# Optimization experiments

Hardware: AMD Instinct MI355X
Metric: run time of the kernel (lower is better)

## Reference

```python
import jax, jax.numpy as jnp
import numpy as np

C_IN, C_P1, C_G1, N_OUT = 512, 256, 256, 6
B, H, W = 256, 19, 19


def mish(x):
    return x * jnp.tanh(jax.nn.softplus(x))


def setup_inputs() -> dict:
    key = jax.random.key(0)
    ks = jax.random.split(key, 8)
    x = jax.random.normal(ks[0], (B, C_IN, H, W), dtype=jnp.float32)
    mask = jnp.ones((B, 1, H, W), dtype=jnp.float32)
    conv1p_w = jax.random.normal(ks[1], (C_P1, C_IN), dtype=jnp.float32) * (1.0 / np.sqrt(C_IN))
    conv1g_w = jax.random.normal(ks[2], (C_G1, C_IN), dtype=jnp.float32) * (1.0 / np.sqrt(C_IN))
    beta_g = jnp.zeros((C_G1,), dtype=jnp.float32)
    linear_g_w = jax.random.normal(ks[3], (C_P1, 3 * C_G1), dtype=jnp.float32) * (1.0 / np.sqrt(3 * C_G1))
    beta2 = jnp.zeros((C_P1,), dtype=jnp.float32)
    conv2p_w = jax.random.normal(ks[4], (N_OUT, C_P1), dtype=jnp.float32) * (0.3 / np.sqrt(C_P1))
    return {"x": x, "mask": mask, "conv1p_w": conv1p_w, "conv1g_w": conv1g_w,
            "beta_g": beta_g, "linear_g_w": linear_g_w, "beta2": beta2, "conv2p_w": conv2p_w}


def reference(x, mask, conv1p_w, conv1g_w, beta_g, linear_g_w, beta2, conv2p_w):
    # 1x1 convs are channel GEMMs
    outp = jnp.einsum('bchw,oc->bohw', x, conv1p_w)              # [B, C_P1, H, W]
    outg = jnp.einsum('bchw,oc->bohw', x, conv1g_w)              # [B, C_G1, H, W]
    # BiasMask (scale=None) + Mish
    outg = mish((outg + beta_g[None, :, None, None]) * mask)
    # KataGPool: mean, scaled mean, max (masked)
    mask_sum_hw = jnp.sum(mask, axis=(2, 3), keepdims=True)      # [B,1,1,1]
    layer_mean = jnp.sum(outg * mask, axis=(2, 3), keepdims=True) / mask_sum_hw
    layer_max = jnp.max(outg + (mask - 1.0), axis=(2, 3), keepdims=True)
    sqrt_off = (jnp.sqrt(mask_sum_hw) - 14.0) / 10.0
    pooled = jnp.concatenate([layer_mean, layer_mean * sqrt_off, layer_max], axis=1)  # [B, 3*C_G1, 1, 1]
    pooled = pooled[:, :, 0, 0]                                  # [B, 3*C_G1]
    g = pooled @ linear_g_w.T                                    # [B, C_P1]
    # broadcast-add, BiasMask, Mish
    outp = mish((outp + g[:, :, None, None] + beta2[None, :, None, None]) * mask)
    # final 1x1 conv + invalid-move penalty
    outp = jnp.einsum('bchw,oc->bohw', outp, conv2p_w)           # [B, 6, H, W]
    outp = outp - (1.0 - mask) * 5000.0
    return outp.reshape(outp.shape[0], outp.shape[1], -1)        # [B, 6, H*W]
```

## Files before the change

kernel.cpp:

```cpp
#include <hip/hip_runtime.h>
#include <math.h>

#define BATCH 256
#define CIN   512
#define CP    256
#define HW    361
#define NOUT  6

typedef short bf16x8 __attribute__((ext_vector_type(8)));
typedef float f32x4  __attribute__((ext_vector_type(4)));

__device__ __forceinline__ short f2bf(float f) {
    unsigned u = __float_as_uint(f);
    u += 0x7fffu + ((u >> 16) & 1u);
    return (short)(u >> 16);
}
__device__ __forceinline__ float bf2f(short s) {
    return __uint_as_float(((unsigned)(unsigned short)s) << 16);
}
__device__ __forceinline__ float mish_f(float v) {
    float u = __expf(v);
    float a = 1.f + u;
    float w = a * a;
    float r = v * (w - 1.f) * __builtin_amdgcn_rcpf(w + 1.f);
    return (v > 30.f) ? v : r;
}
__device__ __forceinline__ void gl_lds16(const void* g, void* l) {
    __builtin_amdgcn_global_load_lds(
        (const __attribute__((address_space(1))) void*)g,
        (__attribute__((address_space(3))) void*)l, 16, 0, 0);
}

__global__ __launch_bounds__(256) void k0_weights(
    const float* __restrict__ w1p, const float* __restrict__ w1g,
    short* __restrict__ wT)
{
    int g = blockIdx.x * 256 + threadIdx.x;
    int half = g >> 14;
    int kb   = (g >> 10) & 15;
    int row  = (g >> 2) & 255;
    int s    = g & 3;
    int sc   = s ^ ((row >> 1) & 3);
    const float* src = (half == 0) ? (w1p + (size_t)row * CIN)
                                   : (w1g + (size_t)row * CIN);
    int c = kb * 32 + sc * 8;
    float f[8];
    *(float4*)(f)     = *(const float4*)(src + c);
    *(float4*)(f + 4) = *(const float4*)(src + c + 4);
    bf16x8 v;
    #pragma unroll
    for (int i = 0; i < 8; ++i) v[i] = f2bf(f[i]);
    *(bf16x8*)((char*)wT + (size_t)half * 262144 + kb * 16384 + row * 64 + s * 16) = v;
}

__global__ __launch_bounds__(512, 4) void k1_conv1(
    const float* __restrict__ x, const short* __restrict__ wT,
    const float* __restrict__ mask, const float* __restrict__ beta_g,
    short* __restrict__ outp_pre, float* __restrict__ psum, float* __restrict__ pmax)
{
    int orig = blockIdx.x;
    int newid = (orig & 7) * 192 + (orig >> 3);
    int half = newid & 1;
    int nb = newid >> 1;
    int n = nb % 3;
    int b = nb / 3;

    const int tid = threadIdx.x;
    const int lane = tid & 63, wid = tid >> 6;
    const int wm = wid >> 1, wn = wid & 1;
    const int lc = lane & 15, lg = lane >> 4;
    const int hw0 = n * 128;

    __shared__ __align__(16) short As[3][8192];
    __shared__ __align__(16) short Bs[2][4096];
    __shared__ float maskS[128], betaS[256];
    float* redS = (float*)(&As[0][0]);
    float* redM = redS + 512;

    if (tid < 128) {
        int hwg = hw0 + tid;
        maskS[tid] = (hwg < HW) ? mask[b * HW + hwg] : 0.f;
    }
    if (tid < 256) betaS[tid] = beta_g[tid];
    asm volatile("s_waitcnt vmcnt(0) lgkmcnt(0)" ::: "memory");
    __builtin_amdgcn_sched_barrier(0);

    const int brow = tid & 127;
    const int bs   = tid >> 7;
    const int bsc  = bs ^ ((brow >> 1) & 3);
    const int hwg  = hw0 + brow;
    const bool bvalid = hwg < HW;
    const float* xb = x + ((size_t)b * CIN + bsc * 8) * HW + hwg;
    char* bDstBase = (char*)Bs;

    const char* aSrc = (const char*)wT + (size_t)half * 262144 + tid * 16;
    char* aDst = (char*)As + tid * 16;

    int aOff[4], bOff[4];
    #pragma unroll
    for (int mf = 0; mf < 4; ++mf) {
        int r = wm * 64 + mf * 16 + lc;
        aOff[mf] = r * 64 + ((lg ^ ((r >> 1) & 3)) * 16);
    }
    #pragma unroll
    for (int nf = 0; nf < 4; ++nf) {
        int r = wn * 64 + nf * 16 + lc;
        bOff[nf] = r * 64 + ((lg ^ ((r >> 1) & 3)) * 16);
    }

    float regB[8];
    #pragma unroll
    for (int i = 0; i < 8; ++i) regB[i] = 0.f;

    f32x4 acc[4][4];
    #pragma unroll
    for (int i = 0; i < 4; ++i)
        #pragma unroll
        for (int j = 0; j < 4; ++j)
            acc[i][j] = (f32x4){0.f, 0.f, 0.f, 0.f};

#define BLOAD(kb)                                                          \
    do {                                                                   \
        const float* src_ = xb + (size_t)(kb) * 32 * HW;                   \
        _Pragma("unroll")                                                  \
        for (int i_ = 0; i_ < 8; ++i_) {                                   \
            regB[i_] = bvalid ? src_[(size_t)i_ * HW] : 0.f;               \
        }                                                                  \
    } while (0)

#define BWRITE(buf)                                                        \
    do {                                                                   \
        bf16x8 o_;                                                         \
        _Pragma("unroll")                                                  \
        for (int i_ = 0; i_ < 8; ++i_) o_[i_] = f2bf(regB[i_]);            \
        *(bf16x8*)(bDstBase + (buf) * 8192 + brow * 64 + bs * 16) = o_;    \
    } while (0)

#define ALOAD(buf, kb)                                                     \
    do {                                                                   \
        gl_lds16(aSrc + (kb) * 16384,        aDst + (buf) * 16384);        \
        gl_lds16(aSrc + (kb) * 16384 + 8192, aDst + (buf) * 16384 + 8192); \
    } while (0)

    BLOAD(0); ALOAD(0, 0);
    asm volatile("s_waitcnt vmcnt(2)" ::: "memory");
    __builtin_amdgcn_sched_barrier(0);
    BWRITE(0);
    BLOAD(1); ALOAD(1, 1);
    asm volatile("s_waitcnt vmcnt(10)" ::: "memory");
    __builtin_amdgcn_sched_barrier(0);
    asm volatile("s_waitcnt lgkmcnt(0)" ::: "memory");
    __builtin_amdgcn_s_barrier();
    __builtin_amdgcn_sched_barrier(0);

    #pragma unroll
    for (int t = 0; t < 16; ++t) {
        const int bufA = t % 3;
        const int bufB = t & 1;
        const char* ab = (const char*)As + bufA * 16384;
        const char* bb = (const char*)Bs + bufB * 8192;

        bf16x8 aF[4], bF[4];
        #pragma unroll
        for (int mf = 0; mf < 4; ++mf) aF[mf] = *(const bf16x8*)(ab + aOff[mf]);
        #pragma unroll
        for (int nf = 0; nf < 4; ++nf) bF[nf] = *(const bf16x8*)(bb + bOff[nf]);

        if (t < 15) {
            asm volatile("s_waitcnt vmcnt(2)" ::: "memory");
            __builtin_amdgcn_sched_barrier(0);
            BWRITE((t + 1) & 1);
        }
        if (t < 14) {
            BLOAD(t + 2); ALOAD((t + 2) % 3, t + 2);
        }

        __builtin_amdgcn_s_setprio(1);
        #pragma unroll
        for (int mf = 0; mf < 4; ++mf)
            #pragma unroll
            for (int nf = 0; nf < 4; ++nf)
                acc[mf][nf] = __builtin_amdgcn_mfma_f32_16x16x32_bf16(
                    aF[mf], bF[nf], acc[mf][nf], 0, 0, 0);
        __builtin_amdgcn_s_setprio(0);

        if (t < 14) {
            asm volatile("s_waitcnt vmcnt(10)" ::: "memory");
        } else if (t == 14) {
            asm volatile("s_waitcnt vmcnt(0)" ::: "memory");
        }
        if (t < 15) {
            __builtin_amdgcn_sched_barrier(0);
            asm volatile("s_waitcnt lgkmcnt(0)" ::: "memory");
            __builtin_amdgcn_s_barrier();
            __builtin_amdgcn_sched_barrier(0);
        }
    }
    __syncthreads();

    if (half == 0) {
        #pragma unroll
        for (int mf = 0; mf < 4; ++mf) {
            int ch = wm * 64 + mf * 16 + lg * 4;
            #pragma unroll
            for (int nf = 0; nf < 4; ++nf) {
                int hw = hw0 + wn * 64 + nf * 16 + lc;
                if (hw < HW) {
                    #pragma unroll
                    for (int j = 0; j < 4; ++j)
                        outp_pre[((size_t)(b * CP + ch + j)) * HW + hw] = f2bf(acc[mf][nf][j]);
                }
            }
        }
    } else {
        #pragma unroll
        for (int mf = 0; mf < 4; ++mf) {
            #pragma unroll
            for (int j = 0; j < 4; ++j) {
                int rloc = wm * 64 + mf * 16 + lg * 4 + j;
                float beta = betaS[rloc];
                float s = 0.f, mx = -INFINITY;
                #pragma unroll
                for (int nf = 0; nf < 4; ++nf) {
                    int cl = wn * 64 + nf * 16 + lc;
                    int hw = hw0 + cl;
                    float mv = maskS[cl];
                    float val = mish_f((acc[mf][nf][j] + beta) * mv);
                    if (hw < HW) {
                        s += val * mv;
                        mx = fmaxf(mx, val + mv - 1.f);
                    }
                }
                #pragma unroll
                for (int off = 1; off < 16; off <<= 1) {
                    s += __shfl_xor(s, off, 64);
                    mx = fmaxf(mx, __shfl_xor(mx, off, 64));
                }
                if (lc == 0) { redS[rloc * 2 + wn] = s; redM[rloc * 2 + wn] = mx; }
            }
        }
        __syncthreads();
        if (tid < 256) {
            float s = redS[tid * 2] + redS[tid * 2 + 1];
            float mx = fmaxf(redM[tid * 2], redM[tid * 2 + 1]);
            psum[((size_t)(b * CP + tid)) * 3 + n] = s;
            pmax[((size_t)(b * CP + tid)) * 3 + n] = mx;
        }
    }
#undef BLOAD
#undef BWRITE
#undef ALOAD
}

__global__ __launch_bounds__(256) void k2_pool_linear(
    const float* __restrict__ mask, const float* __restrict__ psum,
    const float* __restrict__ pmax, const float* __restrict__ lw,
    float* __restrict__ g_out)
{
    int b = blockIdx.x, t = threadIdx.x;
    __shared__ float pooled[768];
    __shared__ float msr[4];

    float s = 0.f;
    for (int i = t; i < HW; i += 256) s += mask[b * HW + i];
    #pragma unroll
    for (int off = 1; off < 64; off <<= 1) s += __shfl_xor(s, off, 64);
    if ((t & 63) == 0) msr[t >> 6] = s;
    __syncthreads();
    float msum = msr[0] + msr[1] + msr[2] + msr[3];

    {
        int c = t;
        const float* ps = psum + (size_t)(b * CP + c) * 3;
        const float* pm = pmax + (size_t)(b * CP + c) * 3;
        float s3 = ps[0] + ps[1] + ps[2];
        float m3 = fmaxf(fmaxf(pm[0], pm[1]), pm[2]);
        float mean = s3 / msum;
        float sq = (sqrtf(msum) - 14.f) * 0.1f;
        pooled[c] = mean; pooled[256 + c] = mean * sq; pooled[512 + c] = m3;
    }
    __syncthreads();
    {
        int o = t;
        const float4* wrow = (const float4*)(lw + (size_t)o * 768);
        float acc = 0.f;
        #pragma unroll 8
        for (int j = 0; j < 192; ++j) {
            float4 w4 = wrow[j];
            float4 p4 = *(const float4*)&pooled[j * 4];
            acc += p4.x * w4.x + p4.y * w4.y + p4.z * w4.z + p4.w * w4.w;
        }
        g_out[b * CP + o] = acc;
    }
}

__global__ __launch_bounds__(256) void k3_final(
    const short* __restrict__ outp_pre, const float* __restrict__ mask,
    const float* __restrict__ g_out, const float* __restrict__ beta2,
    const float* __restrict__ w2, float* __restrict__ out)
{
    int ht = blockIdx.x, b = blockIdx.y;
    int t = threadIdx.x;
    __shared__ float w2S[NOUT * 256];
    __shared__ float gbS[256];
    __shared__ float part[NOUT][256];

    for (int i = t; i < NOUT * 256; i += 256) w2S[i] = w2[i];
    gbS[t] = g_out[b * CP + t] + beta2[t];
    __syncthreads();

    int hw = t & 63, cg = t >> 6;
    int hwg = ht * 64 + hw;
    bool valid = hwg < HW;
    float maskv = valid ? mask[b * HW + hwg] : 0.f;

    float acc[NOUT] = {0.f, 0.f, 0.f, 0.f, 0.f, 0.f};
    const short* src = outp_pre + ((size_t)(b * CP + cg * 64)) * HW + hwg;
    #pragma unroll 4
    for (int ci = 0; ci < 64; ++ci) {
        float v = valid ? bf2f(src[(size_t)ci * HW]) : 0.f;
        float mm = mish_f((v + gbS[cg * 64 + ci]) * maskv);
        #pragma unroll
        for (int o = 0; o < NOUT; ++o) acc[o] += mm * w2S[o * 256 + cg * 64 + ci];
    }
    #pragma unroll
    for (int o = 0; o < NOUT; ++o) part[o][t] = acc[o];
    __syncthreads();

    for (int idx = t; idx < NOUT * 64; idx += 256) {
        int o = idx >> 6, h2 = idx & 63;
        int hg = ht * 64 + h2;
        if (hg < HW) {
            float mv = mask[b * HW + hg];
            float sum = part[o][h2] + part[o][64 + h2] + part[o][128 + h2] + part[o][192 + h2];
            out[((size_t)(b * NOUT + o)) * HW + hg] = sum - (1.f - mv) * 5000.f;
        }
    }
}

extern "C" void kernel_launch(void* const* d_in, const int* in_sizes, int n_in,
                              void* d_out, int out_size, void* d_ws, size_t ws_size,
                              hipStream_t stream) {
    const float* x     = (const float*)d_in[0];
    const float* mask  = (const float*)d_in[1];
    const float* w1p   = (const float*)d_in[2];
    const float* w1g   = (const float*)d_in[3];
    const float* betag = (const float*)d_in[4];
    const float* lw    = (const float*)d_in[5];
    const float* beta2 = (const float*)d_in[6];
    const float* w2    = (const float*)d_in[7];
    float* out = (float*)d_out;

    char* ws = (char*)d_ws;
    short* outp_pre = (short*)(ws);
    short* wT       = (short*)(ws + 47316992);
    float* psum     = (float*)(ws + 47841280);
    float* pmax     = (float*)(ws + 48627712);
    float* g_out    = (float*)(ws + 49414144);

    hipLaunchKernelGGL(k0_weights, dim3(128), dim3(256), 0, stream, w1p, w1g, wT);
    hipLaunchKernelGGL(k1_conv1, dim3(1536), dim3(512), 0, stream,
                       x, wT, mask, betag, outp_pre, psum, pmax);
    hipLaunchKernelGGL(k2_pool_linear, dim3(BATCH), dim3(256), 0, stream,
                       mask, psum, pmax, lw, g_out);
    hipLaunchKernelGGL(k3_final, dim3(6, BATCH), dim3(256), 0, stream,
                       outp_pre, mask, g_out, beta2, w2, out);
    (void)in_sizes; (void)n_in; (void)out_size; (void)ws_size;
}
```

Baseline: 159.3 us.

## Triple-buffer B tile and move B convert-write after MFMAs

Expands the B (activation) LDS buffer from double to triple buffering to match A. The bf16 convert-and-store of the next B tile and the next global B load now happen after the MFMA block instead of before it, so MFMAs issue without waiting on the global load. The LDS swizzle moves from the global source address to the LDS destination offset, so global reads become unswizzled and contiguous per channel. It uses more shared memory, which could lower occupancy, and the vmcnt accounting is reworked around the new order.

```diff
diff --git a/kernel.cpp b/kernel.cpp
--- a/kernel.cpp
+++ b/kernel.cpp
@@ -72,14 +72,14 @@
     const int hw0 = n * 128;
 
     __shared__ __align__(16) short As[3][8192];
-    __shared__ __align__(16) short Bs[2][4096];
+    __shared__ __align__(16) short Bs[3][4096];
     __shared__ float maskS[128], betaS[256];
     float* redS = (float*)(&As[0][0]);
     float* redM = redS + 512;
 
     if (tid < 128) {
-        int hwg = hw0 + tid;
-        maskS[tid] = (hwg < HW) ? mask[b * HW + hwg] : 0.f;
+        int hwg_ = hw0 + tid;
+        maskS[tid] = (hwg_ < HW) ? mask[b * HW + hwg_] : 0.f;
     }
     if (tid < 256) betaS[tid] = beta_g[tid];
     asm volatile("s_waitcnt vmcnt(0) lgkmcnt(0)" ::: "memory");
@@ -87,10 +87,10 @@
 
     const int brow = tid & 127;
     const int bs   = tid >> 7;
-    const int bsc  = bs ^ ((brow >> 1) & 3);
     const int hwg  = hw0 + brow;
     const bool bvalid = hwg < HW;
-    const float* xb = x + ((size_t)b * CIN + bsc * 8) * HW + hwg;
+    const float* xb = x + ((size_t)b * CIN + bs * 8) * HW + hwg;
+    const int bDstOff = brow * 64 + ((bs ^ ((brow >> 1) & 3)) * 16);
     char* bDstBase = (char*)Bs;
 
     const char* aSrc = (const char*)wT + (size_t)half * 262144 + tid * 16;
@@ -133,7 +133,7 @@
         bf16x8 o_;                                                         \
         _Pragma("unroll")                                                  \
         for (int i_ = 0; i_ < 8; ++i_) o_[i_] = f2bf(regB[i_]);            \
-        *(bf16x8*)(bDstBase + (buf) * 8192 + brow * 64 + bs * 16) = o_;    \
+        *(bf16x8*)(bDstBase + (buf) * 8192 + bDstOff) = o_;                \
     } while (0)
 
 #define ALOAD(buf, kb)                                                     \
@@ -142,23 +142,21 @@
         gl_lds16(aSrc + (kb) * 16384 + 8192, aDst + (buf) * 16384 + 8192); \
     } while (0)
 
-    BLOAD(0); ALOAD(0, 0);
+    ALOAD(0, 0); BLOAD(0);
+    ALOAD(1, 1);
     asm volatile("s_waitcnt vmcnt(2)" ::: "memory");
     __builtin_amdgcn_sched_barrier(0);
     BWRITE(0);
-    BLOAD(1); ALOAD(1, 1);
-    asm volatile("s_waitcnt vmcnt(10)" ::: "memory");
-    __builtin_amdgcn_sched_barrier(0);
+    BLOAD(1);
     asm volatile("s_waitcnt lgkmcnt(0)" ::: "memory");
     __builtin_amdgcn_s_barrier();
     __builtin_amdgcn_sched_barrier(0);
 
     #pragma unroll
     for (int t = 0; t < 16; ++t) {
-        const int bufA = t % 3;
-        const int bufB = t & 1;
-        const char* ab = (const char*)As + bufA * 16384;
-        const char* bb = (const char*)Bs + bufB * 8192;
+        const int buf = t % 3;
+        const char* ab = (const char*)As + buf * 16384;
+        const char* bb = (const char*)Bs + buf * 8192;
 
         bf16x8 aF[4], bF[4];
         #pragma unroll
@@ -166,14 +164,7 @@
         #pragma unroll
         for (int nf = 0; nf < 4; ++nf) bF[nf] = *(const bf16x8*)(bb + bOff[nf]);
 
-        if (t < 15) {
-            asm volatile("s_waitcnt vmcnt(2)" ::: "memory");
-            __builtin_amdgcn_sched_barrier(0);
-            BWRITE((t + 1) & 1);
-        }
-        if (t < 14) {
-            BLOAD(t + 2); ALOAD((t + 2) % 3, t + 2);
-        }
+        if (t < 14) { ALOAD((t + 2) % 3, t + 2); }
 
         __builtin_amdgcn_s_setprio(1);
         #pragma unroll
@@ -185,12 +176,16 @@
         __builtin_amdgcn_s_setprio(0);
 
         if (t < 14) {
-            asm volatile("s_waitcnt vmcnt(10)" ::: "memory");
+            asm volatile("s_waitcnt vmcnt(2)" ::: "memory");
+            __builtin_amdgcn_sched_barrier(0);
+            BWRITE((t + 1) % 3);
+            BLOAD(t + 2);
         } else if (t == 14) {
             asm volatile("s_waitcnt vmcnt(0)" ::: "memory");
+            __builtin_amdgcn_sched_barrier(0);
+            BWRITE(15 % 3);
         }
         if (t < 15) {
-            __builtin_amdgcn_sched_barrier(0);
             asm volatile("s_waitcnt lgkmcnt(0)" ::: "memory");
             __builtin_amdgcn_s_barrier();
             __builtin_amdgcn_sched_barrier(0);
```

Result: faster. 142.9 us (-10.3%).
